# Optimization experiments

Hardware: AMD Instinct MI355X
Metric: run time of the kernel (lower is better)

Reference implementation:

```python
import jax, jax.numpy as jnp
import numpy as np

NUM_HEADS = 16
THETA = 10000.0


def _apply_rope(x, pos):
    # x: [b, h, t, d_k], pos: [t] int
    d = x.shape[-1]
    inv_freq = THETA ** (-jnp.arange(0, d, 2, dtype=jnp.float32) / d)  # [d/2]
    ang = pos.astype(jnp.float32)[:, None] * inv_freq                  # [t, d/2]
    cos, sin = jnp.cos(ang), jnp.sin(ang)
    x1, x2 = x[..., ::2], x[..., 1::2]
    r1 = x1 * cos - x2 * sin
    r2 = x1 * sin + x2 * cos
    return jnp.stack([r1, r2], axis=-1).reshape(x.shape)


def setup_inputs() -> dict:
    key = jax.random.key(0)
    k1, k2, k3 = jax.random.split(key, 3)
    b, t, dm = 4, 2048, 2048
    in_features = jax.random.normal(k1, (b, t, dm), dtype=jnp.float32)
    token_positions = jnp.arange(t, dtype=jnp.int64)
    W_qkv = jax.random.normal(k2, (3 * dm, dm), dtype=jnp.float32) * 0.02
    W_o = jax.random.normal(k3, (dm, dm), dtype=jnp.float32) * 0.02
    return {"in_features": in_features, "token_positions": token_positions,
            "W_qkv": W_qkv, "W_o": W_o}


def reference(in_features, token_positions, W_qkv, W_o):
    b, t, dm = in_features.shape
    h = NUM_HEADS
    dk = dm // h
    # fused QKV projection (Linear: y = x W^T)
    qkv = in_features @ W_qkv.T                       # [b, t, 3*dm]
    q, k, v = jnp.split(qkv, 3, axis=-1)
    def to_heads(x):
        return x.reshape(b, t, h, dk).transpose(0, 2, 1, 3)  # [b, h, t, dk]
    q, k, v = to_heads(q), to_heads(k), to_heads(v)
    q = _apply_rope(q, token_positions)
    k = _apply_rope(k, token_positions)
    # causal SDPA
    scale = 1.0 / np.sqrt(dk).astype(np.float32)
    scores = jnp.einsum('bhqd,bhkd->bhqk', q, k) * scale
    causal = jnp.tril(jnp.ones((t, t), dtype=bool))
    scores = jnp.where(causal, scores, jnp.finfo(scores.dtype).min)
    attn = jax.nn.softmax(scores, axis=-1)
    out = jnp.einsum('bhqk,bhkd->bhqd', attn, v)      # [b, h, t, dk]
    out = out.transpose(0, 2, 1, 3).reshape(b, t, dm)
    return out @ W_o.T
```

## Files before the change

kernel.cpp:

```cpp
#include <hip/hip_runtime.h>

typedef unsigned short u16;
typedef __attribute__((ext_vector_type(8))) short s8v;
typedef __attribute__((ext_vector_type(8))) __bf16 bf8;
typedef __attribute__((ext_vector_type(4))) float f4v;

#define GLB(p) ((const __attribute__((address_space(1))) void*)(p))
#define LDS(p) ((__attribute__((address_space(3))) void*)(p))

static __device__ __forceinline__ float b2f(u16 u) {
    union { unsigned int i; float f; } v; v.i = ((unsigned int)u) << 16; return v.f;
}
static __device__ __forceinline__ u16 f2b(float f) {
    union { float f; unsigned int i; } v; v.f = f;
    v.i += 0x7fffu + ((v.i >> 16) & 1u);
    return (u16)(v.i >> 16);
}

__global__ __launch_bounds__(256) void k_conv(const float* __restrict__ in,
                                              u16* __restrict__ out, int n4) {
    int i = blockIdx.x * 256 + threadIdx.x;
    if (i >= n4) return;
    float4 v = ((const float4*)in)[i];
    union { u16 u[4]; unsigned long long ll; } o;
    o.u[0] = f2b(v.x); o.u[1] = f2b(v.y); o.u[2] = f2b(v.z); o.u[3] = f2b(v.w);
    ((unsigned long long*)out)[i] = o.ll;
}

template<int MODE>
__global__ __launch_bounds__(512, 2) void k_gemm_bt(
    const u16* __restrict__ A, const u16* __restrict__ B,
    int K, int N, int gx,
    u16* __restrict__ Qb, u16* __restrict__ Kb, u16* __restrict__ Vt,
    float* __restrict__ Cf)
{
    extern __shared__ __align__(16) u16 Ls[];

    const int t    = threadIdx.x;
    const int lane = t & 63;
    const int wid  = t >> 6;
    const int wm = wid >> 2, wn = wid & 3;
    const int la = lane & 15, lb = lane >> 4;

    const int bid = (int)blockIdx.x;
    const int id2 = (bid & 7) * ((int)gridDim.x >> 3) + (bid >> 3);
    const int bx = id2 % gx, by = id2 / gx;
    const long arow0 = (long)by * 256;
    const long brow0 = (long)bx * 256;

    const int sr = t >> 3;
    const int sg = (t & 7) ^ (sr & 7);
    const u16* Asrc = A + (arow0 + sr) * (long)K + sg * 8;
    const u16* Bsrc = B + (brow0 + sr) * (long)K + sg * 8;
    const long K64 = 64 * (long)K, K128 = 128 * (long)K;
    u16* ldst = Ls + t * 8;

#define STG(q_, op_, h_, kt_) do {                                              \
        const u16* s_ = ((op_) ? Bsrc : Asrc) + (h_) * K128 + (long)(kt_) * 64; \
        u16* d_ = ldst + (q_) * 32768 + (op_) * 16384 + (h_) * 8192;            \
        __builtin_amdgcn_global_load_lds(GLB(s_),       LDS(d_),        16, 0, 0); \
        __builtin_amdgcn_global_load_lds(GLB(s_ + K64), LDS(d_ + 4096), 16, 0, 0); \
    } while (0)
#define RD(off) (*(const bf8*)(Ls + (off)))

    f4v acc[8][4];
#pragma unroll
    for (int m = 0; m < 8; m++)
#pragma unroll
        for (int n = 0; n < 4; n++) acc[m][n] = (f4v){0.f, 0.f, 0.f, 0.f};

    const int r7 = la & 7;
    const int gA0 = (lb ^ r7) * 8;
    const int gA1 = ((lb ^ r7) ^ 4) * 8;
    const int aRow = wm * 8192 + la * 64;
    const int bRow = 16384 + (wn >> 1) * 8192 + ((wn & 1) * 64 + la) * 64;

    const int NKT = K >> 6;
    STG(0, 0, 0, 0); STG(0, 0, 1, 0); STG(0, 1, 0, 0); STG(0, 1, 1, 0);
    asm volatile("s_waitcnt vmcnt(0)" ::: "memory");
    __builtin_amdgcn_s_barrier();

    for (int X = 0; X < NKT; ++X) {
        const int D = (X & 1) << 15;
        const int q = (X + 1) & 1;
        const int S = (X + 1 < NKT) ? X + 1 : NKT - 1;
        bf8 aR[4][2], b0[2][2], b1[2][2];

#pragma unroll
        for (int mi = 0; mi < 4; mi++) {
            aR[mi][0] = RD(D + aRow + mi * 1024 + gA0);
            aR[mi][1] = RD(D + aRow + mi * 1024 + gA1);
        }
#pragma unroll
        for (int nl = 0; nl < 2; nl++) {
            b0[nl][0] = RD(D + bRow + nl * 1024 + gA0);
            b0[nl][1] = RD(D + bRow + nl * 1024 + gA1);
        }
        STG(q, 0, 0, S); STG(q, 0, 1, S); STG(q, 1, 0, S); STG(q, 1, 1, S);
        __builtin_amdgcn_s_barrier();
        __builtin_amdgcn_s_setprio(1);
#pragma unroll
        for (int mi = 0; mi < 4; mi++)
#pragma unroll
            for (int nl = 0; nl < 2; nl++) {
                acc[mi][nl] = __builtin_amdgcn_mfma_f32_16x16x32_bf16(aR[mi][0], b0[nl][0], acc[mi][nl], 0, 0, 0);
                acc[mi][nl] = __builtin_amdgcn_mfma_f32_16x16x32_bf16(aR[mi][1], b0[nl][1], acc[mi][nl], 0, 0, 0);
            }
        __builtin_amdgcn_s_setprio(0);

#pragma unroll
        for (int nl = 0; nl < 2; nl++) {
            b1[nl][0] = RD(D + bRow + (2 + nl) * 1024 + gA0);
            b1[nl][1] = RD(D + bRow + (2 + nl) * 1024 + gA1);
        }
        __builtin_amdgcn_s_barrier();
        __builtin_amdgcn_s_setprio(1);
#pragma unroll
        for (int mi = 0; mi < 4; mi++)
#pragma unroll
            for (int nl = 0; nl < 2; nl++) {
                acc[mi][2 + nl] = __builtin_amdgcn_mfma_f32_16x16x32_bf16(aR[mi][0], b1[nl][0], acc[mi][2 + nl], 0, 0, 0);
                acc[mi][2 + nl] = __builtin_amdgcn_mfma_f32_16x16x32_bf16(aR[mi][1], b1[nl][1], acc[mi][2 + nl], 0, 0, 0);
            }
        __builtin_amdgcn_s_setprio(0);

#pragma unroll
        for (int mi = 0; mi < 4; mi++) {
            aR[mi][0] = RD(D + aRow + (4 + mi) * 1024 + gA0);
            aR[mi][1] = RD(D + aRow + (4 + mi) * 1024 + gA1);
        }
        __builtin_amdgcn_s_barrier();
        __builtin_amdgcn_s_setprio(1);
#pragma unroll
        for (int mi = 0; mi < 4; mi++)
#pragma unroll
            for (int nl = 0; nl < 2; nl++) {
                acc[4 + mi][2 + nl] = __builtin_amdgcn_mfma_f32_16x16x32_bf16(aR[mi][0], b1[nl][0], acc[4 + mi][2 + nl], 0, 0, 0);
                acc[4 + mi][2 + nl] = __builtin_amdgcn_mfma_f32_16x16x32_bf16(aR[mi][1], b1[nl][1], acc[4 + mi][2 + nl], 0, 0, 0);
            }
        __builtin_amdgcn_s_setprio(0);

        asm volatile("s_waitcnt vmcnt(0)" ::: "memory");
        __builtin_amdgcn_s_barrier();
        __builtin_amdgcn_s_setprio(1);
#pragma unroll
        for (int mi = 0; mi < 4; mi++)
#pragma unroll
            for (int nl = 0; nl < 2; nl++) {
                acc[4 + mi][nl] = __builtin_amdgcn_mfma_f32_16x16x32_bf16(aR[mi][0], b0[nl][0], acc[4 + mi][nl], 0, 0, 0);
                acc[4 + mi][nl] = __builtin_amdgcn_mfma_f32_16x16x32_bf16(aR[mi][1], b0[nl][1], acc[4 + mi][nl], 0, 0, 0);
            }
        __builtin_amdgcn_s_setprio(0);
    }
#undef STG
#undef RD

    if (MODE == 1) {
#pragma unroll
        for (int mi = 0; mi < 8; mi++)
#pragma unroll
            for (int ni = 0; ni < 4; ni++) {
                const long grow0 = arow0 + wm * 128 + mi * 16 + lb * 4;
                const int  gcol  = (int)brow0 + wn * 64 + ni * 16 + la;
#pragma unroll
                for (int i = 0; i < 4; i++)
                    Cf[(grow0 + i) * (long)N + gcol] = acc[mi][ni][i];
            }
        return;
    }

    __syncthreads();
    const int part = (int)(brow0 >> 11);
    const int colp = (int)brow0 & 2047;
    const int h0   = colp >> 7;
    const int bidx = (int)(arow0 >> 11);
    const int t0   = (int)arow0 & 2047;

    if (part == 2) {
#pragma unroll
        for (int mi = 0; mi < 8; mi++)
#pragma unroll
            for (int ni = 0; ni < 4; ni++) {
                const int tlb = wm * 128 + mi * 16 + lb * 4;
                const int dl  = wn * 64 + ni * 16 + la;
#pragma unroll
                for (int i2 = 0; i2 < 2; i2++) {
                    unsigned int pk = (unsigned int)f2b(acc[mi][ni][i2 * 2])
                                    | ((unsigned int)f2b(acc[mi][ni][i2 * 2 + 1]) << 16);
                    *(unsigned int*)(Ls + dl * 264 + tlb + i2 * 2) = pk;
                }
            }
        __syncthreads();
        const int w = wid;
#pragma unroll
        for (int j = 0; j < 16; j++) {
            const int dl = j * 16 + w * 2 + (lane >> 5);
            const int c  = lane & 31;
            bf8 v = *(const bf8*)(Ls + dl * 264 + c * 8);
            const long bh = (long)(bidx * 16 + h0 + (dl >> 7));
            *(bf8*)(Vt + (bh << 18) + ((long)(dl & 127) << 11) + t0 + c * 8) = v;
        }
    } else {
        u16* dst = (part == 0) ? Qb : Kb;
#pragma unroll
        for (int mi = 0; mi < 8; mi++)
#pragma unroll
            for (int ni = 0; ni < 4; ni++) {
                const int tlb = wm * 128 + mi * 16 + lb * 4;
                const int dl  = wn * 64 + ni * 16 + la;
#pragma unroll
                for (int i = 0; i < 4; i++)
                    Ls[(tlb + i) * 264 + dl] = f2b(acc[mi][ni][i]);
            }
        __syncthreads();
#pragma unroll
        for (int j = 0; j < 16; j++) {
            const int R  = j * 32 + (t >> 4);
            const int tl = R >> 1, hh = R & 1, c = t & 15;
            bf8 v = *(const bf8*)(Ls + tl * 264 + hh * 128 + c * 8);
            const long bh = (long)(bidx * 16 + h0 + hh);
            *(bf8*)(dst + ((bh << 11) + t0 + tl) * 128 + c * 8) = v;
        }
    }
}

__global__ __launch_bounds__(256) void k_rope(u16* __restrict__ Qb, u16* __restrict__ Kb,
                                              const int* __restrict__ pos) {
    const int idx = blockIdx.x * 256 + threadIdx.x;
    const int j  = idx & 63;
    const int t  = (idx >> 6) & 2047;
    const int bh = (idx >> 17) & 63;
    u16* P = (idx >> 23) ? Kb : Qb;
    const long off = ((((long)bh << 11) + t) << 7) + 2 * j;
    unsigned int raw = *(unsigned int*)(P + off);
    float x1 = b2f((u16)(raw & 0xffffu));
    float x2 = b2f((u16)(raw >> 16));
    float invf = exp2f((float)j * -0.20762050593046014f);
    float ang = (float)pos[t] * invf;
    float sn, cs;
    sincosf(ang, &sn, &cs);
    unsigned int o = (unsigned int)f2b(x1 * cs - x2 * sn)
                   | ((unsigned int)f2b(x1 * sn + x2 * cs) << 16);
    *(unsigned int*)(P + off) = o;
}

__global__ __launch_bounds__(512) void k_attn(const u16* __restrict__ Qb,
                                              const u16* __restrict__ Kb,
                                              const u16* __restrict__ Vt,
                                              u16* __restrict__ Ob)
{
    __shared__ __align__(16) u16 Ks[2][32 * 128];
    __shared__ __align__(16) u16 Vs[2][64 * 64];
    __shared__ __align__(16) u16 Pl[8][32 * 32];

    const int tid  = threadIdx.x;
    const int lane = tid & 63;
    const int w    = tid >> 6;
    const int la = lane & 15, lb = lane >> 4;
    const int qg = 7 - ((int)blockIdx.x >> 6);
    const int bh = blockIdx.x & 63;
    const long base = (long)bh << 18;
    const int qt = qg * 8 + w;
    const int q0 = qt * 32;
    const int tiles_w = qt + 1;
    const int NT = qg * 8 + 8;
    const float scale = 0.08838834764831845f;

    bf8 qf[2][4];
#pragma unroll
    for (int m = 0; m < 2; m++)
#pragma unroll
        for (int kb = 0; kb < 4; kb++)
            qf[m][kb] = *(const bf8*)(Qb + base + (long)(q0 + m * 16 + la) * 128 + kb * 32 + lb * 8);

    f4v o[2][8];
#pragma unroll
    for (int m = 0; m < 2; m++)
#pragma unroll
        for (int n = 0; n < 8; n++) o[m][n] = (f4v){0.f, 0.f, 0.f, 0.f};
    float lst[2][4];
#pragma unroll
    for (int m = 0; m < 2; m++)
#pragma unroll
        for (int i = 0; i < 4; i++) lst[m][i] = 0.f;

    char* Pb = (char*)(Pl[w]);

    const int ko = tid * 16;
    const int kr = ko >> 8, kc = (ko & 255) ^ ((kr & 7) << 4);
    const int vo = tid * 16;
    const int vR = vo >> 7, vc = (vo & 127) ^ ((vR & 7) << 4);
    const int vd = 2 * vR + (vc >> 6), vt = (vc & 63) >> 1;

#define STAGE(buf, jt_) do {                                                        \
        const int kv0_ = (jt_) * 32;                                               \
        __builtin_amdgcn_global_load_lds(                                          \
            GLB(Kb + base + (long)(kv0_ + kr) * 128 + (kc >> 1)),                  \
            LDS((u16*)Ks[buf] + tid * 8), 16, 0, 0);                               \
        __builtin_amdgcn_global_load_lds(                                          \
            GLB(Vt + base + ((long)vd << 11) + kv0_ + vt),                         \
            LDS((u16*)Vs[buf] + tid * 8), 16, 0, 0);                               \
    } while (0)

    STAGE(0, 0);

    for (int jt = 0; jt < NT; ++jt) {
        const int buf = jt & 1;
        __syncthreads();
        if (jt + 1 < NT) STAGE(buf ^ 1, jt + 1);

        if (jt < tiles_w) {
            const char* KsB = (const char*)Ks[buf];
            const char* VsB = (const char*)Vs[buf];

            f4v s[2][2];
            s[0][0] = s[0][1] = s[1][0] = s[1][1] = (f4v){0.f, 0.f, 0.f, 0.f};
#pragma unroll
            for (int n = 0; n < 2; n++) {
                const int row = n * 16 + la;
#pragma unroll
                for (int kb = 0; kb < 4; kb++) {
                    bf8 kf = *(const bf8*)(KsB + row * 256 + ((kb * 64 + lb * 16) ^ ((row & 7) << 4)));
                    s[0][n] = __builtin_amdgcn_mfma_f32_16x16x32_bf16(qf[0][kb], kf, s[0][n], 0, 0, 0);
                    s[1][n] = __builtin_amdgcn_mfma_f32_16x16x32_bf16(qf[1][kb], kf, s[1][n], 0, 0, 0);
                }
            }

            bf8 vf[8];
#pragma unroll
            for (int nO = 0; nO < 8; nO++) {
                const int R = nO * 8 + (la >> 1);
                vf[nO] = *(const bf8*)(VsB + R * 128 + (((la & 1) * 64 + lb * 16) ^ ((R & 7) << 4)));
            }

            const bool diag = (jt == qt);
            float p[2][2][4];
#pragma unroll
            for (int m = 0; m < 2; m++)
#pragma unroll
                for (int n = 0; n < 2; n++)
#pragma unroll
                    for (int i = 0; i < 4; i++) {
                        float v = __expf(fmaf(s[m][n][i], scale, -8.0f));
                        if (diag && (n * 16 + la) > (m * 16 + lb * 4 + i)) v = 0.f;
                        p[m][n][i] = v;
                        lst[m][i] += v;
                    }

#pragma unroll
            for (int m = 0; m < 2; m++)
#pragma unroll
                for (int n = 0; n < 2; n++)
#pragma unroll
                    for (int i = 0; i < 4; i++) {
                        const int row = m * 16 + lb * 4 + i;
                        const int colb = (n * 16 + la) * 2;
                        *(u16*)(Pb + row * 64 + (colb ^ ((row & 3) << 4))) = f2b(p[m][n][i]);
                    }
            bf8 pa[2];
#pragma unroll
            for (int am = 0; am < 2; am++) {
                const int row = am * 16 + la;
                pa[am] = *(const bf8*)(Pb + row * 64 + ((lb * 16) ^ ((row & 3) << 4)));
            }
#pragma unroll
            for (int nO = 0; nO < 8; nO++) {
                o[0][nO] = __builtin_amdgcn_mfma_f32_16x16x32_bf16(pa[0], vf[nO], o[0][nO], 0, 0, 0);
                o[1][nO] = __builtin_amdgcn_mfma_f32_16x16x32_bf16(pa[1], vf[nO], o[1][nO], 0, 0, 0);
            }
        }
        __syncthreads();
    }
#undef STAGE

    float linv[2][4];
#pragma unroll
    for (int m = 0; m < 2; m++)
#pragma unroll
        for (int i = 0; i < 4; i++) {
            float l = lst[m][i];
            l += __shfl_xor(l, 1);
            l += __shfl_xor(l, 2);
            l += __shfl_xor(l, 4);
            l += __shfl_xor(l, 8);
            linv[m][i] = 1.0f / l;
        }

    const int b = bh >> 4, h = bh & 15;
#pragma unroll
    for (int m = 0; m < 2; m++)
#pragma unroll
        for (int nO = 0; nO < 8; nO++)
#pragma unroll
            for (int i = 0; i < 4; i++) {
                const int row = q0 + m * 16 + lb * 4 + i;
                const int d = nO * 16 + la;
                Ob[((long)(b * 2048 + row) << 11) + h * 128 + d] = f2b(o[m][nO][i] * linv[m][i]);
            }
}

extern "C" void kernel_launch(void* const* d_in, const int* in_sizes, int n_in,
                              void* d_out, int out_size, void* d_ws, size_t ws_size,
                              hipStream_t stream)
{
    const float* X    = (const float*)d_in[0];
    const int*   pos  = (const int*)d_in[1];
    const float* Wqkv = (const float*)d_in[2];
    const float* Wo   = (const float*)d_in[3];
    float* out = (float*)d_out;

    char* ws = (char*)d_ws;
    u16* Xb    = (u16*)(ws + 0);
    u16* Wqkvb = (u16*)(ws + 33554432);
    u16* Wob   = (u16*)(ws + 58720256);
    u16* Qb    = (u16*)(ws + 67108864);
    u16* Kb    = (u16*)(ws + 100663296);
    u16* Vt    = (u16*)(ws + 134217728);
    u16* Ob    = (u16*)(ws + 167772160);

    k_conv<<<16384, 256, 0, stream>>>(X, Xb, 4194304);
    k_conv<<<12288, 256, 0, stream>>>(Wqkv, Wqkvb, 3145728);
    k_conv<<<4096, 256, 0, stream>>>(Wo, Wob, 1048576);
    k_gemm_bt<0><<<768, 512, 139392, stream>>>(Xb, Wqkvb, 2048, 6144, 24, Qb, Kb, Vt, nullptr);
    k_rope<<<65536, 256, 0, stream>>>(Qb, Kb, pos);
    k_attn<<<512, 512, 0, stream>>>(Qb, Kb, Vt, Ob);
    k_gemm_bt<1><<<256, 512, 139392, stream>>>(Ob, Wob, 2048, 2048, 8, nullptr, nullptr, nullptr, out);
}
```

Baseline: 436.2 us.

## Fuse RoPE into QKV GEMM epilogue and merge conversion kernels

Applies rotary embedding to Q and K inside the QKV GEMM epilogue, before writing to global memory, and deletes the separate k_rope kernel that re-read and re-wrote Q and K. The three fp32-to-bf16 conversion launches become one launch. Dynamic shared memory sizes for both GEMM launches are also reduced. RoPE now uses the fast __sincosf intrinsic in place of sincosf, which may lose some accuracy at large angles.

```diff
diff --git a/kernel.cpp b/kernel.cpp
--- a/kernel.cpp
+++ b/kernel.cpp
@@ -17,14 +17,21 @@
     return (u16)(v.i >> 16);
 }
 
-__global__ __launch_bounds__(256) void k_conv(const float* __restrict__ in,
-                                              u16* __restrict__ out, int n4) {
+__global__ __launch_bounds__(256) void k_conv(const float* __restrict__ X,
+                                              const float* __restrict__ Wq,
+                                              const float* __restrict__ Wo,
+                                              u16* __restrict__ Xb,
+                                              u16* __restrict__ Wqb,
+                                              u16* __restrict__ Wob) {
     int i = blockIdx.x * 256 + threadIdx.x;
-    if (i >= n4) return;
-    float4 v = ((const float4*)in)[i];
+    const float* in; u16* out; int off;
+    if (i < 4194304)      { in = X;  out = Xb;  off = i; }
+    else if (i < 7340032) { in = Wq; out = Wqb; off = i - 4194304; }
+    else                  { in = Wo; out = Wob; off = i - 7340032; }
+    float4 v = ((const float4*)in)[off];
     union { u16 u[4]; unsigned long long ll; } o;
     o.u[0] = f2b(v.x); o.u[1] = f2b(v.y); o.u[2] = f2b(v.z); o.u[3] = f2b(v.w);
-    ((unsigned long long*)out)[i] = o.ll;
+    ((unsigned long long*)out)[off] = o.ll;
 }
 
 template<int MODE>
@@ -32,7 +39,7 @@
     const u16* __restrict__ A, const u16* __restrict__ B,
     int K, int N, int gx,
     u16* __restrict__ Qb, u16* __restrict__ Kb, u16* __restrict__ Vt,
-    float* __restrict__ Cf)
+    float* __restrict__ Cf, const int* __restrict__ pos)
 {
     extern __shared__ __align__(16) u16 Ls[];
 
@@ -191,10 +198,9 @@
                 }
             }
         __syncthreads();
-        const int w = wid;
 #pragma unroll
         for (int j = 0; j < 16; j++) {
-            const int dl = j * 16 + w * 2 + (lane >> 5);
+            const int dl = j * 16 + wid * 2 + (lane >> 5);
             const int c  = lane & 31;
             bf8 v = *(const bf8*)(Ls + dl * 264 + c * 8);
             const long bh = (long)(bidx * 16 + h0 + (dl >> 7));
@@ -213,35 +219,31 @@
                     Ls[(tlb + i) * 264 + dl] = f2b(acc[mi][ni][i]);
             }
         __syncthreads();
+        const int c = t & 15;
+        float invf[4];
+#pragma unroll
+        for (int p2 = 0; p2 < 4; p2++)
+            invf[p2] = exp2f((float)(c * 4 + p2) * -0.20762050593046014f);
 #pragma unroll
         for (int j = 0; j < 16; j++) {
             const int R  = j * 32 + (t >> 4);
-            const int tl = R >> 1, hh = R & 1, c = t & 15;
-            bf8 v = *(const bf8*)(Ls + tl * 264 + hh * 128 + c * 8);
+            const int tl = R >> 1, hh = R & 1;
+            s8v v = *(const s8v*)(Ls + tl * 264 + hh * 128 + c * 8);
+            const float pf = (float)pos[t0 + tl];
+            union { u16 u[8]; s8v v; } ov;
+#pragma unroll
+            for (int p2 = 0; p2 < 4; p2++) {
+                float x1 = b2f((u16)v[2 * p2]);
+                float x2 = b2f((u16)v[2 * p2 + 1]);
+                float sn, cs;
+                __sincosf(pf * invf[p2], &sn, &cs);
+                ov.u[2 * p2]     = f2b(x1 * cs - x2 * sn);
+                ov.u[2 * p2 + 1] = f2b(x1 * sn + x2 * cs);
+            }
             const long bh = (long)(bidx * 16 + h0 + hh);
-            *(bf8*)(dst + ((bh << 11) + t0 + tl) * 128 + c * 8) = v;
+            *(s8v*)(dst + ((bh << 11) + t0 + tl) * 128 + c * 8) = ov.v;
         }
     }
-}
-
-__global__ __launch_bounds__(256) void k_rope(u16* __restrict__ Qb, u16* __restrict__ Kb,
-                                              const int* __restrict__ pos) {
-    const int idx = blockIdx.x * 256 + threadIdx.x;
-    const int j  = idx & 63;
-    const int t  = (idx >> 6) & 2047;
-    const int bh = (idx >> 17) & 63;
-    u16* P = (idx >> 23) ? Kb : Qb;
-    const long off = ((((long)bh << 11) + t) << 7) + 2 * j;
-    unsigned int raw = *(unsigned int*)(P + off);
-    float x1 = b2f((u16)(raw & 0xffffu));
-    float x2 = b2f((u16)(raw >> 16));
-    float invf = exp2f((float)j * -0.20762050593046014f);
-    float ang = (float)pos[t] * invf;
-    float sn, cs;
-    sincosf(ang, &sn, &cs);
-    unsigned int o = (unsigned int)f2b(x1 * cs - x2 * sn)
-                   | ((unsigned int)f2b(x1 * sn + x2 * cs) << 16);
-    *(unsigned int*)(P + off) = o;
 }
 
 __global__ __launch_bounds__(512) void k_attn(const u16* __restrict__ Qb,
@@ -418,11 +420,8 @@
     u16* Vt    = (u16*)(ws + 134217728);
     u16* Ob    = (u16*)(ws + 167772160);
 
-    k_conv<<<16384, 256, 0, stream>>>(X, Xb, 4194304);
-    k_conv<<<12288, 256, 0, stream>>>(Wqkv, Wqkvb, 3145728);
-    k_conv<<<4096, 256, 0, stream>>>(Wo, Wob, 1048576);
-    k_gemm_bt<0><<<768, 512, 139392, stream>>>(Xb, Wqkvb, 2048, 6144, 24, Qb, Kb, Vt, nullptr);
-    k_rope<<<65536, 256, 0, stream>>>(Qb, Kb, pos);
+    k_conv<<<32768, 256, 0, stream>>>(X, Wqkv, Wo, Xb, Wqkvb, Wob);
+    k_gemm_bt<0><<<768, 512, 135168, stream>>>(Xb, Wqkvb, 2048, 6144, 24, Qb, Kb, Vt, nullptr, pos);
     k_attn<<<512, 512, 0, stream>>>(Qb, Kb, Vt, Ob);
-    k_gemm_bt<1><<<256, 512, 139392, stream>>>(Ob, Wob, 2048, 2048, 8, nullptr, nullptr, nullptr, out);
-}
+    k_gemm_bt<1><<<256, 512, 131072, stream>>>(Ob, Wob, 2048, 2048, 8, nullptr, nullptr, nullptr, out, nullptr);
+}
```

Result: faster. 405.5 us (-7.1%).
